# Optimization experiments

Measured on AMD Instinct MI355X. Metric: run time of the kernel, lower is better.

## Reference

```python
import jax, jax.numpy as jnp
import numpy as np

D = 1024
NHEAD = 16
HEAD_DIM = D // NHEAD


def setup_inputs() -> dict:
    key = jax.random.key(0)
    ks = jax.random.split(key, 7)
    B, L = 4, 2048
    q = jax.random.normal(ks[0], (B, L, D), dtype=jnp.float32)
    k = jax.random.normal(ks[1], (B, L, D), dtype=jnp.float32)
    v = jax.random.normal(ks[2], (B, L, D), dtype=jnp.float32)
    # packed QKV projection, as in nn.MultiheadAttention (in_proj_weight: [3d, d])
    scale = 1.0 / np.sqrt(D)
    in_proj_w = jax.random.uniform(ks[3], (3 * D, D), dtype=jnp.float32, minval=-scale, maxval=scale)
    in_proj_b = jnp.zeros((3 * D,), dtype=jnp.float32)
    out_w = jax.random.uniform(ks[4], (D, D), dtype=jnp.float32, minval=-scale, maxval=scale)
    out_b = jnp.zeros((D,), dtype=jnp.float32)
    return {"q": q, "k": k, "v": v, "in_proj_w": in_proj_w, "in_proj_b": in_proj_b,
            "out_w": out_w, "out_b": out_b}


def reference(q, k, v, in_proj_w, in_proj_b, out_w, out_b):
    # FP32 MHA, need_weights=True (average over heads), eval mode (dropout inactive).
    B, Lq, d = q.shape
    Lk = k.shape[1]
    # packed in-projection: rows [0:d] -> Q, [d:2d] -> K, [2d:3d] -> V
    qp = q @ in_proj_w[:d].T + in_proj_b[:d]
    kp = k @ in_proj_w[d:2 * d].T + in_proj_b[d:2 * d]
    vp = v @ in_proj_w[2 * d:].T + in_proj_b[2 * d:]
    # split heads: [B, H, L, hd]
    qp = qp.reshape(B, Lq, NHEAD, HEAD_DIM).transpose(0, 2, 1, 3)
    kp = kp.reshape(B, Lk, NHEAD, HEAD_DIM).transpose(0, 2, 1, 3)
    vp = vp.reshape(B, Lk, NHEAD, HEAD_DIM).transpose(0, 2, 1, 3)
    scores = jnp.einsum('bhqd,bhkd->bhqk', qp, kp) / jnp.sqrt(jnp.float32(HEAD_DIM))
    attn = jax.nn.softmax(scores, axis=-1)          # [B, H, Lq, Lk]
    ctx = jnp.einsum('bhqk,bhkd->bhqd', attn, vp)    # [B, H, Lq, hd]
    ctx = ctx.transpose(0, 2, 1, 3).reshape(B, Lq, d)
    out = ctx @ out_w.T + out_b                      # [B, Lq, d]
    weights = attn.mean(axis=1)                      # average over heads -> [B, Lq, Lk]
    return out, weights
```

## Files before the change

kernel.cpp:

```cpp
#include <hip/hip_runtime.h>
#include <hip/hip_bf16.h>

#define D_ 1024
#define NH 16
#define HD 64
#define B_ 4
#define L_ 2048
#define N_ (B_*L_)
#define BH_ (B_*NH)
#define QSCALE_ 0.18033688011112042f

typedef __bf16 bf16_t;
typedef __bf16 bf16x4 __attribute__((ext_vector_type(4)));
typedef __bf16 bf16x8 __attribute__((ext_vector_type(8)));
typedef float f32x4 __attribute__((ext_vector_type(4)));

typedef const __attribute__((address_space(1))) char gas_t;
typedef __attribute__((address_space(3))) char las_t;

__device__ __forceinline__ f32x4 mfma_bf16(bf16x8 a, bf16x8 b, f32x4 c) {
    return __builtin_amdgcn_mfma_f32_16x16x32_bf16(a, b, c, 0, 0, 0);
}

__device__ __forceinline__ bf16x8 cvt8_f32(const float* __restrict__ p) {
    const float4* p4 = reinterpret_cast<const float4*>(p);
    float4 a = p4[0], b = p4[1];
    bf16x8 r;
    r[0] = (bf16_t)a.x; r[1] = (bf16_t)a.y; r[2] = (bf16_t)a.z; r[3] = (bf16_t)a.w;
    r[4] = (bf16_t)b.x; r[5] = (bf16_t)b.y; r[6] = (bf16_t)b.z; r[7] = (bf16_t)b.w;
    return r;
}

__device__ __forceinline__ bf16x8 ld8_bf16(const bf16_t* __restrict__ p) {
    return *reinterpret_cast<const bf16x8*>(p);
}

__global__ __launch_bounds__(256) void k_cvt_all(
    const float* __restrict__ s0, const float* __restrict__ s1,
    const float* __restrict__ s2, const float* __restrict__ sw,
    const float* __restrict__ so,
    bf16_t* __restrict__ d0, bf16_t* __restrict__ d1, bf16_t* __restrict__ d2,
    bf16_t* __restrict__ dw, bf16_t* __restrict__ dow)
{
    const int n8  = N_ * D_ / 8;
    const int n8w = 3 * D_ * D_ / 8;
    const int n8o = D_ * D_ / 8;
    const int tot = 3 * n8 + n8w + n8o;
    int i = blockIdx.x * blockDim.x + threadIdx.x;
    int stride = gridDim.x * blockDim.x;
    for (; i < tot; i += stride) {
        const float* s; bf16_t* d; int off;
        if (i < 3 * n8) {
            int seg = i >> 20; off = i & (n8 - 1);
            s = (seg == 0) ? s0 : ((seg == 1) ? s1 : s2);
            d = (seg == 0) ? d0 : ((seg == 1) ? d1 : d2);
        } else if (i < 3 * n8 + n8w) {
            off = i - 3 * n8; s = sw; d = dw;
        } else {
            off = i - 3 * n8 - n8w; s = so; d = dow;
        }
        *reinterpret_cast<bf16x8*>(d + (size_t)off * 8) = cvt8_f32(s + (size_t)off * 8);
    }
}

__global__ __launch_bounds__(256) void k_gemm_qkv(
    const bf16_t* __restrict__ qb, const bf16_t* __restrict__ kb,
    const bf16_t* __restrict__ vb, const bf16_t* __restrict__ wb,
    const float* __restrict__ bias,
    bf16_t* __restrict__ qp, bf16_t* __restrict__ kp, bf16_t* __restrict__ vpT)
{
    __shared__ __align__(16) char lds[2][8192];
    int tid  = threadIdx.x;
    int lane = tid & 63, w = tid >> 6;
    int r = lane & 15, g = lane >> 4;
    int wr = w >> 1, wc = w & 1;

    int bid = blockIdx.x;
    int swz = (bid & 7) * 192 + (bid >> 3);
    int tm = swz / 24, tn = swz % 24;
    int sec = tn >> 3;
    int ctl = (tn & 7) * 128;

    const bf16_t* A = (sec == 0) ? qb : ((sec == 1) ? kb : vb);
    const bf16_t* Ab = A + (size_t)tm * 128 * 1024;
    const bf16_t* Bb = wb + (size_t)sec * D_ * D_ + (size_t)ctl * 1024;

    f32x4 z = {0.f, 0.f, 0.f, 0.f};
    f32x4 acc[4][4];
    #pragma unroll
    for (int m = 0; m < 4; ++m)
        #pragma unroll
        for (int n = 0; n < 4; ++n) acc[m][n] = z;

    for (int k0 = 0; k0 < 1024; k0 += 32) {
        #pragma unroll
        for (int i = 0; i < 2; ++i) {
            int o = i * 4096 + tid * 16;
            int row = o >> 6;
            int lchunk = ((o >> 4) & 3) ^ (row & 3);
            const bf16_t* gA = Ab + (size_t)row * 1024 + k0 + lchunk * 8;
            const bf16_t* gB = Bb + (size_t)row * 1024 + k0 + lchunk * 8;
            char* lpA = &lds[0][0] + i * 4096 + w * 1024;
            char* lpB = &lds[1][0] + i * 4096 + w * 1024;
            __builtin_amdgcn_global_load_lds((gas_t*)gA, (las_t*)lpA, 16, 0, 0);
            __builtin_amdgcn_global_load_lds((gas_t*)gB, (las_t*)lpB, 16, 0, 0);
        }
        __syncthreads();

        bf16x8 af[4], bf_[4];
        #pragma unroll
        for (int m = 0; m < 4; ++m) {
            int R = wr * 64 + m * 16 + r;
            af[m] = *reinterpret_cast<const bf16x8*>(
                &lds[0][0] + R * 64 + (((g ^ (R & 3)) << 4)));
        }
        #pragma unroll
        for (int n = 0; n < 4; ++n) {
            int R = wc * 64 + n * 16 + r;
            bf_[n] = *reinterpret_cast<const bf16x8*>(
                &lds[1][0] + R * 64 + (((g ^ (R & 3)) << 4)));
        }
        #pragma unroll
        for (int m = 0; m < 4; ++m)
            #pragma unroll
            for (int n = 0; n < 4; ++n)
                acc[m][n] = mfma_bf16(af[m], bf_[n], acc[m][n]);
        __syncthreads();
    }

    #pragma unroll
    for (int m = 0; m < 4; ++m)
        #pragma unroll
        for (int n = 0; n < 4; ++n)
            #pragma unroll
            for (int i = 0; i < 4; ++i) {
                int row = tm * 128 + wr * 64 + m * 16 + g * 4 + i;
                int col = ctl + wc * 64 + n * 16 + r;
                float val = acc[m][n][i] + bias[sec * 1024 + col];
                int bb = row >> 11, ln = row & 2047;
                int h = col >> 6, dd = col & 63;
                if (sec == 0)
                    qp[(((size_t)(bb * NH + h)) * L_ + ln) * HD + dd] =
                        (bf16_t)(val * QSCALE_);
                else if (sec == 1)
                    kp[(((size_t)(bb * NH + h)) * L_ + ln) * HD + dd] = (bf16_t)val;
                else
                    vpT[(((size_t)(bb * NH + h)) * HD + dd) * L_ + ln] = (bf16_t)val;
            }
}

__global__ __launch_bounds__(256) void k_gemm_out(
    const bf16_t* __restrict__ A, const bf16_t* __restrict__ Bm,
    const float* __restrict__ bias, float* __restrict__ dst)
{
    __shared__ __align__(16) char lds[2][8192];
    int tid  = threadIdx.x;
    int lane = tid & 63, w = tid >> 6;
    int r = lane & 15, g = lane >> 4;
    int wr = w >> 1, wc = w & 1;

    int bid = blockIdx.x;
    int swz = (bid & 7) * 64 + (bid >> 3);
    int tm = swz >> 3, tn = swz & 7;

    const bf16_t* Ab = A  + (size_t)tm * 128 * 1024;
    const bf16_t* Bb = Bm + (size_t)tn * 128 * 1024;

    f32x4 z = {0.f, 0.f, 0.f, 0.f};
    f32x4 acc[4][4];
    #pragma unroll
    for (int m = 0; m < 4; ++m)
        #pragma unroll
        for (int n = 0; n < 4; ++n) acc[m][n] = z;

    for (int k0 = 0; k0 < 1024; k0 += 32) {
        #pragma unroll
        for (int i = 0; i < 2; ++i) {
            int o = i * 4096 + tid * 16;
            int row = o >> 6;
            int lchunk = ((o >> 4) & 3) ^ (row & 3);
            const bf16_t* gA = Ab + (size_t)row * 1024 + k0 + lchunk * 8;
            const bf16_t* gB = Bb + (size_t)row * 1024 + k0 + lchunk * 8;
            char* lpA = &lds[0][0] + i * 4096 + w * 1024;
            char* lpB = &lds[1][0] + i * 4096 + w * 1024;
            __builtin_amdgcn_global_load_lds((gas_t*)gA, (las_t*)lpA, 16, 0, 0);
            __builtin_amdgcn_global_load_lds((gas_t*)gB, (las_t*)lpB, 16, 0, 0);
        }
        __syncthreads();

        bf16x8 af[4], bf_[4];
        #pragma unroll
        for (int m = 0; m < 4; ++m) {
            int R = wr * 64 + m * 16 + r;
            af[m] = *reinterpret_cast<const bf16x8*>(
                &lds[0][0] + R * 64 + (((g ^ (R & 3)) << 4)));
        }
        #pragma unroll
        for (int n = 0; n < 4; ++n) {
            int R = wc * 64 + n * 16 + r;
            bf_[n] = *reinterpret_cast<const bf16x8*>(
                &lds[1][0] + R * 64 + (((g ^ (R & 3)) << 4)));
        }
        #pragma unroll
        for (int m = 0; m < 4; ++m)
            #pragma unroll
            for (int n = 0; n < 4; ++n)
                acc[m][n] = mfma_bf16(af[m], bf_[n], acc[m][n]);
        __syncthreads();
    }

    #pragma unroll
    for (int m = 0; m < 4; ++m)
        #pragma unroll
        for (int n = 0; n < 4; ++n)
            #pragma unroll
            for (int i = 0; i < 4; ++i) {
                int row = tm * 128 + wr * 64 + m * 16 + g * 4 + i;
                int col = tn * 128 + wc * 64 + n * 16 + r;
                dst[(size_t)row * 1024 + col] = acc[m][n][i] + bias[col];
            }
}

__global__ __launch_bounds__(256, 3) void k_attn(
    const bf16_t* __restrict__ qp, const bf16_t* __restrict__ kp,
    const bf16_t* __restrict__ vpT,
    bf16_t* __restrict__ ctx, float* __restrict__ lInvOut)
{
    __shared__ __align__(16) char sK[2][8192];
    __shared__ __align__(16) char sV[2][8192];
    __shared__ __align__(16) char sP[4][4096];

    int tid  = threadIdx.x;
    int w    = tid >> 6;
    int lane = tid & 63;
    int r = lane & 15, g = lane >> 4;
    int bh = blockIdx.x & 63;
    int qg = blockIdx.x >> 6;
    int qbase = qg * 128 + w * 32;

    const bf16_t* qpb = qp  + (size_t)bh * L_ * HD;
    const bf16_t* kpb = kp  + (size_t)bh * L_ * HD;
    const bf16_t* vtb = vpT + (size_t)bh * HD * L_;

    bf16x8 bq[2][2];
    #pragma unroll
    for (int qt = 0; qt < 2; ++qt)
        #pragma unroll
        for (int ds = 0; ds < 2; ++ds)
            bq[qt][ds] = ld8_bf16(qpb + (size_t)(qbase + qt * 16 + r) * HD + ds * 32 + g * 8);

    bf16x8 ones;
    #pragma unroll
    for (int i = 0; i < 8; ++i) ones[i] = (bf16_t)1.0f;

    f32x4 z = {0.f, 0.f, 0.f, 0.f};
    f32x4 acc[2][4];
    #pragma unroll
    for (int qt = 0; qt < 2; ++qt)
        #pragma unroll
        for (int dt = 0; dt < 4; ++dt) acc[qt][dt] = z;
    f32x4 acc_l[2];
    acc_l[0] = z; acc_l[1] = z;

    char* Pw = &sP[w][0];

    int srow = tid >> 3;
    int slc  = (tid & 7) ^ (srow & 7);
    const bf16_t* gK0 = kpb + (size_t)srow * HD + slc * 8;
    const bf16_t* gV0 = vtb + (size_t)srow * L_ + slc * 8;

    auto stage = [&](int buf, int k0) {
        const bf16_t* gK = gK0 + (size_t)k0 * HD;
        const bf16_t* gV = gV0 + k0;
        #pragma unroll
        for (int i = 0; i < 2; ++i) {
            __builtin_amdgcn_global_load_lds((gas_t*)(gK + (size_t)i * 32 * HD),
                (las_t*)(&sK[buf][0] + i * 4096 + tid * 16), 16, 0, 0);
            __builtin_amdgcn_global_load_lds((gas_t*)(gV + (size_t)i * 32 * L_),
                (las_t*)(&sV[buf][0] + i * 4096 + tid * 16), 16, 0, 0);
        }
    };

    stage(0, 0);
    __syncthreads();
    int buf = 0;

    for (int kt = 0; kt < 32; ++kt) {
        if (kt + 1 < 32) stage(buf ^ 1, (kt + 1) * 64);

        const char* Kb = &sK[buf][0];
        const char* Vb = &sV[buf][0];

        f32x4 sT[4][2];
        __builtin_amdgcn_s_setprio(1);
        #pragma unroll
        for (int ktile = 0; ktile < 4; ++ktile) {
            bf16x8 a0 = *reinterpret_cast<const bf16x8*>(
                Kb + (ktile * 16 + r) * 128 + (((g    ) ^ (r & 7)) << 4));
            bf16x8 a1 = *reinterpret_cast<const bf16x8*>(
                Kb + (ktile * 16 + r) * 128 + (((4 + g) ^ (r & 7)) << 4));
            #pragma unroll
            for (int qt = 0; qt < 2; ++qt) {
                f32x4 t = mfma_bf16(a0, bq[qt][0], z);
                sT[ktile][qt] = mfma_bf16(a1, bq[qt][1], t);
            }
        }
        __builtin_amdgcn_s_setprio(0);

        #pragma unroll
        for (int qt = 0; qt < 2; ++qt) {
            #pragma unroll
            for (int ktile = 0; ktile < 4; ++ktile) {
                bf16x4 pw;
                #pragma unroll
                for (int i = 0; i < 4; ++i)
                    pw[i] = (bf16_t)__builtin_amdgcn_exp2f(sT[ktile][qt][i]);
                *reinterpret_cast<bf16x4*>(Pw + (qt * 16 + r) * 128 +
                    (((2 * ktile + (g >> 1)) ^ (r & 7)) << 4) + ((g & 1) << 3)) = pw;
            }
        }

        bf16x8 pa[2][2];
        #pragma unroll
        for (int qt = 0; qt < 2; ++qt)
            #pragma unroll
            for (int ks = 0; ks < 2; ++ks)
                pa[qt][ks] = *reinterpret_cast<const bf16x8*>(
                    Pw + (qt * 16 + r) * 128 + (((4 * ks + g) ^ (r & 7)) << 4));
        __builtin_amdgcn_s_setprio(1);
        #pragma unroll
        for (int qt = 0; qt < 2; ++qt) {
            acc_l[qt] = mfma_bf16(pa[qt][0], ones, acc_l[qt]);
            acc_l[qt] = mfma_bf16(pa[qt][1], ones, acc_l[qt]);
        }
        #pragma unroll
        for (int dt = 0; dt < 4; ++dt)
            #pragma unroll
            for (int ks = 0; ks < 2; ++ks) {
                bf16x8 bv = *reinterpret_cast<const bf16x8*>(
                    Vb + (dt * 16 + r) * 128 + (((4 * ks + g) ^ (r & 7)) << 4));
                acc[0][dt] = mfma_bf16(pa[0][ks], bv, acc[0][dt]);
                acc[1][dt] = mfma_bf16(pa[1][ks], bv, acc[1][dt]);
            }
        __builtin_amdgcn_s_setprio(0);

        __syncthreads();
        buf ^= 1;
    }

    int bb = bh >> 4, h = bh & 15;
    #pragma unroll
    for (int qt = 0; qt < 2; ++qt) {
        float lq[4];
        #pragma unroll
        for (int i = 0; i < 4; ++i) lq[i] = 1.0f / acc_l[qt][i];
        #pragma unroll
        for (int i = 0; i < 4; ++i) {
            int q = qbase + qt * 16 + 4 * g + i;
            #pragma unroll
            for (int dt = 0; dt < 4; ++dt) {
                float val = acc[qt][dt][i] * lq[i];
                ctx[(((size_t)(bb * L_ + q)) * NH + h) * HD + dt * 16 + r] = (bf16_t)val;
            }
        }
        if (r == 0) {
            #pragma unroll
            for (int i = 0; i < 4; ++i) {
                int q = qbase + qt * 16 + 4 * g + i;
                lInvOut[(size_t)bh * L_ + q] = lq[i];
            }
        }
    }
}

__global__ __launch_bounds__(256, 2) void k_weights(
    const bf16_t* __restrict__ qp, const bf16_t* __restrict__ kp,
    const float* __restrict__ lInv, float* __restrict__ wout)
{
    __shared__ __align__(16) char sQ[2][16384];
    __shared__ __align__(16) char sKt[2][16384];
    __shared__ __align__(16) float sLi[16][128];

    int tid  = threadIdx.x;
    int w    = tid >> 6;
    int lane = tid & 63;
    int r = lane & 15, g = lane >> 4;
    int wr = w >> 1, wc = w & 1;

    int wgid = (blockIdx.x & 7) * 128 + (blockIdx.x >> 3);
    int chunk = wgid >> 7;
    int b  = chunk >> 1;
    int qh = chunk & 1;
    int rem = wgid & 127;
    int qt = qh * 8 + (rem >> 4);
    int kt = rem & 15;
    int q0 = qt * 128, k0 = kt * 128;

    #pragma unroll
    for (int i = 0; i < 2; ++i) {
        int idx = i * 256 + tid;
        int h   = idx >> 5;
        int off = (idx & 31) * 4;
        const float* gl = lInv + ((size_t)(b * NH + h) * L_ + q0 + off);
        __builtin_amdgcn_global_load_lds((gas_t*)gl,
            (las_t*)((char*)&sLi[0][0] + i * 4096 + w * 1024), 16, 0, 0);
    }

    auto stage_qk = [&](int buf, int h) {
        const bf16_t* Qh = qp + ((size_t)(b * NH + h) * L_ + q0) * HD;
        const bf16_t* Kh = kp + ((size_t)(b * NH + h) * L_ + k0) * HD;
        #pragma unroll
        for (int i = 0; i < 4; ++i) {
            int idx = i * 256 + tid;
            int row = idx >> 3;
            int lc  = (idx & 7) ^ (row & 7);
            const bf16_t* gQ = Qh + (size_t)row * HD + lc * 8;
            const bf16_t* gK = Kh + (size_t)row * HD + lc * 8;
            __builtin_amdgcn_global_load_lds((gas_t*)gQ,
                (las_t*)(&sQ[buf][0]  + i * 4096 + w * 1024), 16, 0, 0);
            __builtin_amdgcn_global_load_lds((gas_t*)gK,
                (las_t*)(&sKt[buf][0] + i * 4096 + w * 1024), 16, 0, 0);
        }
    };

    float acc[4][4][4] = {};
    f32x4 z = {0.f, 0.f, 0.f, 0.f};

    stage_qk(0, 0);
    __syncthreads();
    int buf = 0;

    for (int h = 0; h < NH; ++h) {
        if (h + 1 < NH) stage_qk(buf ^ 1, h + 1);

        const char* Qb = &sQ[buf][0];
        const char* Kb = &sKt[buf][0];

        bf16x8 bfrag[4][2];
        #pragma unroll
        for (int nf = 0; nf < 4; ++nf) {
            int R = wc * 64 + nf * 16 + r;
            bfrag[nf][0] = *reinterpret_cast<const bf16x8*>(
                Kb + R * 128 + (((g    ) ^ (R & 7)) << 4));
            bfrag[nf][1] = *reinterpret_cast<const bf16x8*>(
                Kb + R * 128 + (((4 + g) ^ (R & 7)) << 4));
        }
        #pragma unroll
        for (int mf = 0; mf < 4; ++mf) {
            int R = wr * 64 + mf * 16 + r;
            bf16x8 af0 = *reinterpret_cast<const bf16x8*>(
                Qb + R * 128 + (((g    ) ^ (R & 7)) << 4));
            bf16x8 af1 = *reinterpret_cast<const bf16x8*>(
                Qb + R * 128 + (((4 + g) ^ (R & 7)) << 4));
            int qrow = wr * 64 + mf * 16 + g * 4;
            f32x4 liv = *reinterpret_cast<const f32x4*>(&sLi[h][qrow]);
            #pragma unroll
            for (int nf = 0; nf < 4; ++nf) {
                f32x4 t = mfma_bf16(af0, bfrag[nf][0], z);
                t = mfma_bf16(af1, bfrag[nf][1], t);
                #pragma unroll
                for (int i = 0; i < 4; ++i)
                    acc[mf][nf][i] += __builtin_amdgcn_exp2f(t[i]) * liv[i];
            }
        }
        __syncthreads();
        buf ^= 1;
    }

    const float inv_h = 1.0f / (float)NH;
    #pragma unroll
    for (int mf = 0; mf < 4; ++mf)
        #pragma unroll
        for (int nf = 0; nf < 4; ++nf)
            #pragma unroll
            for (int i = 0; i < 4; ++i) {
                int qidx = q0 + wr * 64 + mf * 16 + g * 4 + i;
                int kidx = k0 + wc * 64 + nf * 16 + r;
                wout[((size_t)(b * L_ + qidx)) * L_ + kidx] = acc[mf][nf][i] * inv_h;
            }
}

extern "C" void kernel_launch(void* const* d_in, const int* in_sizes, int n_in,
                              void* d_out, int out_size, void* d_ws, size_t ws_size,
                              hipStream_t stream) {
    const float* q     = (const float*)d_in[0];
    const float* k     = (const float*)d_in[1];
    const float* v     = (const float*)d_in[2];
    const float* in_w  = (const float*)d_in[3];
    const float* in_b  = (const float*)d_in[4];
    const float* out_w = (const float*)d_in[5];
    const float* out_b = (const float*)d_in[6];

    char* ws = (char*)d_ws;
    bf16_t* xb   = (bf16_t*)(ws);
    bf16_t* wb   = (bf16_t*)(ws + ((size_t)48 << 20));
    bf16_t* owb  = (bf16_t*)(ws + ((size_t)54 << 20));
    bf16_t* qp   = (bf16_t*)(ws + ((size_t)56 << 20));
    bf16_t* kp   = (bf16_t*)(ws + ((size_t)72 << 20));
    bf16_t* vpT  = (bf16_t*)(ws + ((size_t)88 << 20));
    bf16_t* ctx  = (bf16_t*)(ws + ((size_t)104 << 20));
    float*  lBuf = (float*)(ws + ((size_t)120 << 20));

    bf16_t* qb = xb;
    bf16_t* kb = xb + (size_t)N_ * D_;
    bf16_t* vb = xb + (size_t)2 * N_ * D_;

    float* outp = (float*)d_out;
    float* wout = outp + (size_t)N_ * D_;

    k_cvt_all<<<2048, 256, 0, stream>>>(q, k, v, in_w, out_w, qb, kb, vb, wb, owb);

    k_gemm_qkv<<<1536, 256, 0, stream>>>(qb, kb, vb, wb, in_b, qp, kp, vpT);

    k_attn   <<<1024, 256, 0, stream>>>(qp, kp, vpT, ctx, lBuf);
    k_weights<<<1024, 256, 0, stream>>>(qp, kp, lBuf, wout);

    k_gemm_out<<<512, 256, 0, stream>>>(ctx, owb, out_b, outp);
}
```

Baseline: 294.4 us.

## Single-buffer attention K/V staging for higher occupancy and remap QKV GEMM tiles per XCD

```diff
diff --git a/kernel.cpp b/kernel.cpp
--- a/kernel.cpp
+++ b/kernel.cpp
@@ -75,11 +75,13 @@
     int r = lane & 15, g = lane >> 4;
     int wr = w >> 1, wc = w & 1;
 
-    int bid = blockIdx.x;
-    int swz = (bid & 7) * 192 + (bid >> 3);
-    int tm = swz / 24, tn = swz % 24;
-    int sec = tn >> 3;
-    int ctl = (tn & 7) * 128;
+    int bid   = blockIdx.x;
+    int xcd   = bid & 7;
+    int seq   = bid >> 3;
+    int sec   = seq >> 6;
+    int inner = seq & 63;
+    int tm  = xcd * 8 + (inner >> 3);
+    int ctl = (inner & 7) * 128;
 
     const bf16_t* A = (sec == 0) ? qb : ((sec == 1) ? kb : vb);
     const bf16_t* Ab = A + (size_t)tm * 128 * 1024;
@@ -221,13 +223,13 @@
             }
 }
 
-__global__ __launch_bounds__(256, 3) void k_attn(
+__global__ __launch_bounds__(256, 4) void k_attn(
     const bf16_t* __restrict__ qp, const bf16_t* __restrict__ kp,
     const bf16_t* __restrict__ vpT,
     bf16_t* __restrict__ ctx, float* __restrict__ lInvOut)
 {
-    __shared__ __align__(16) char sK[2][8192];
-    __shared__ __align__(16) char sV[2][8192];
+    __shared__ __align__(16) char sK[8192];
+    __shared__ __align__(16) char sV[8192];
     __shared__ __align__(16) char sP[4][4096];
 
     int tid  = threadIdx.x;
@@ -269,36 +271,27 @@
     const bf16_t* gK0 = kpb + (size_t)srow * HD + slc * 8;
     const bf16_t* gV0 = vtb + (size_t)srow * L_ + slc * 8;
 
-    auto stage = [&](int buf, int k0) {
+    for (int kt = 0; kt < 32; ++kt) {
+        int k0 = kt * 64;
         const bf16_t* gK = gK0 + (size_t)k0 * HD;
         const bf16_t* gV = gV0 + k0;
         #pragma unroll
         for (int i = 0; i < 2; ++i) {
             __builtin_amdgcn_global_load_lds((gas_t*)(gK + (size_t)i * 32 * HD),
-                (las_t*)(&sK[buf][0] + i * 4096 + tid * 16), 16, 0, 0);
+                (las_t*)(&sK[0] + i * 4096 + tid * 16), 16, 0, 0);
             __builtin_amdgcn_global_load_lds((gas_t*)(gV + (size_t)i * 32 * L_),
-                (las_t*)(&sV[buf][0] + i * 4096 + tid * 16), 16, 0, 0);
-        }
-    };
-
-    stage(0, 0);
-    __syncthreads();
-    int buf = 0;
-
-    for (int kt = 0; kt < 32; ++kt) {
-        if (kt + 1 < 32) stage(buf ^ 1, (kt + 1) * 64);
-
-        const char* Kb = &sK[buf][0];
-        const char* Vb = &sV[buf][0];
+                (las_t*)(&sV[0] + i * 4096 + tid * 16), 16, 0, 0);
+        }
+        __syncthreads();
 
         f32x4 sT[4][2];
         __builtin_amdgcn_s_setprio(1);
         #pragma unroll
         for (int ktile = 0; ktile < 4; ++ktile) {
             bf16x8 a0 = *reinterpret_cast<const bf16x8*>(
-                Kb + (ktile * 16 + r) * 128 + (((g    ) ^ (r & 7)) << 4));
+                &sK[0] + (ktile * 16 + r) * 128 + (((g    ) ^ (r & 7)) << 4));
             bf16x8 a1 = *reinterpret_cast<const bf16x8*>(
-                Kb + (ktile * 16 + r) * 128 + (((4 + g) ^ (r & 7)) << 4));
+                &sK[0] + (ktile * 16 + r) * 128 + (((4 + g) ^ (r & 7)) << 4));
             #pragma unroll
             for (int qt = 0; qt < 2; ++qt) {
                 f32x4 t = mfma_bf16(a0, bq[qt][0], z);
@@ -338,14 +331,13 @@
             #pragma unroll
             for (int ks = 0; ks < 2; ++ks) {
                 bf16x8 bv = *reinterpret_cast<const bf16x8*>(
-                    Vb + (dt * 16 + r) * 128 + (((4 * ks + g) ^ (r & 7)) << 4));
+                    &sV[0] + (dt * 16 + r) * 128 + (((4 * ks + g) ^ (r & 7)) << 4));
                 acc[0][dt] = mfma_bf16(pa[0][ks], bv, acc[0][dt]);
                 acc[1][dt] = mfma_bf16(pa[1][ks], bv, acc[1][dt]);
             }
         __builtin_amdgcn_s_setprio(0);
 
         __syncthreads();
-        buf ^= 1;
     }
 
     int bb = bh >> 4, h = bh & 15;
```

After: 274.3 us. 1.07x faster.
